# Kernel optimization log

Measured on AMD Instinct MI355X. Metric: run time of the kernel, lower is better.

## Reference

```python
import jax, jax.numpy as jnp
import numpy as np

N_NODES = 30000
N_EDGES = 240000
DIM = 128
HEADS = 2
HID = 2 * DIM          # gat1 per-head out channels = 256
OUT2 = DIM // 2        # gat2 per-head out channels = 64
CLASSES = 20
EPS = 1e-5
NEG_SLOPE = 0.2


def rmsnorm(x, w):
    x32 = x.astype(jnp.float32)
    y = x32 * jax.lax.rsqrt(jnp.mean(x32 * x32, axis=-1, keepdims=True) + EPS)
    return y.astype(x.dtype) * w


def gatv2_conv(x, src, dst, eattr, Wl, bl, Wr, br, We, att, bias, heads, ch):
    """PyG GATv2Conv (concat=True, add_self_loops=True, fill_value='mean')."""
    N = x.shape[0]
    # --- add self loops; self-loop edge_attr = per-node mean of incoming attrs ---
    cnt = jax.ops.segment_sum(jnp.ones((src.shape[0],), x.dtype), dst, num_segments=N)
    loop_attr = jax.ops.segment_sum(eattr, dst, num_segments=N) / jnp.maximum(cnt, 1.0)[:, None]
    loops = jnp.arange(N, dtype=src.dtype)
    src = jnp.concatenate([src, loops])
    dst = jnp.concatenate([dst, loops])
    eattr = jnp.concatenate([eattr, loop_attr], axis=0)
    # --- node transforms ---
    xl = (x @ Wl.T + bl).reshape(N, heads, ch)   # source-side
    xr = (x @ Wr.T + br).reshape(N, heads, ch)   # target-side
    eemb = (eattr @ We.T).reshape(-1, heads, ch)
    # --- edge-wise attention logits (GATv2: LeakyReLU before att dot) ---
    e = jax.nn.leaky_relu(xl[src] + xr[dst] + eemb, negative_slope=NEG_SLOPE)  # [E,H,C]
    logits = jnp.einsum('ehc,hc->eh', e, att)                                   # [E,H]
    # --- segment softmax over destination nodes ---
    m = jnp.full((N, heads), -jnp.inf, logits.dtype).at[dst].max(logits)
    p = jnp.exp(logits - m[dst])
    denom = jax.ops.segment_sum(p, dst, num_segments=N)
    alpha = p / denom[dst]                                                       # [E,H]
    # --- weighted scatter-add of source messages ---
    out = jax.ops.segment_sum(alpha[:, :, None] * xl[src], dst, num_segments=N)  # [N,H,C]
    return out.reshape(N, heads * ch) + bias


def setup_inputs() -> dict:
    key = jax.random.key(0)
    ks = jax.random.split(key, 20)
    d1 = HEADS * HID   # 512
    d2 = HEADS * OUT2  # 128 == DIM
    p = lambda k, shape: (jax.random.normal(k, shape, jnp.float32) * 0.02)
    return {
        'x': jax.random.normal(ks[0], (N_NODES, DIM), jnp.float32),
        'edge_index': jax.random.randint(ks[1], (2, N_EDGES), 0, N_NODES, jnp.int32),
        'edge_attr': jax.random.normal(ks[2], (N_EDGES, 1), jnp.float32),
        'Wl1': p(ks[3], (d1, DIM)), 'bl1': jnp.zeros((d1,), jnp.float32),
        'Wr1': p(ks[4], (d1, DIM)), 'br1': jnp.zeros((d1,), jnp.float32),
        'We1': p(ks[5], (d1, 1)),
        'att1': p(ks[6], (HEADS, HID)),
        'bias1': jnp.zeros((d1,), jnp.float32),
        'Wl2': p(ks[7], (d2, d1)), 'bl2': jnp.zeros((d2,), jnp.float32),
        'Wr2': p(ks[8], (d2, d1)), 'br2': jnp.zeros((d2,), jnp.float32),
        'We2': p(ks[9], (d2, 1)),
        'att2': p(ks[10], (HEADS, OUT2)),
        'bias2': jnp.zeros((d2,), jnp.float32),
        'w_ln1': jnp.ones((d1,), jnp.float32),
        'w_ln3': jnp.ones((d2,), jnp.float32),
        'W_out': p(ks[11], (CLASSES, d2)),
    }


def reference(x, edge_index, edge_attr,
              Wl1, bl1, Wr1, br1, We1, att1, bias1,
              Wl2, bl2, Wr2, br2, We2, att2, bias2,
              w_ln1, w_ln3, W_out):
    src, dst = edge_index[0], edge_index[1]
    h = gatv2_conv(x, src, dst, edge_attr, Wl1, bl1, Wr1, br1, We1, att1, bias1, HEADS, HID)
    h = jax.nn.silu(h)
    h = rmsnorm(h, w_ln1)
    h = gatv2_conv(h, src, dst, edge_attr, Wl2, bl2, Wr2, br2, We2, att2, bias2, HEADS, OUT2)
    h = rmsnorm(h, w_ln3)
    return h @ W_out.T
```

## Files before the change

kernel.cpp:

```cpp
#include <hip/hip_runtime.h>
#include <cstddef>

#define NN   30000
#define NNP  30016
#define NE   240000
#define D1   512
#define D2   128
#define NCLS 20
#define CAP  64
#define CAST_TOT 1025536
#define IDG_TOT  (CAST_TOT + NE)

typedef __attribute__((ext_vector_type(8))) short short8;
typedef __attribute__((ext_vector_type(4))) float f32x4;
typedef __attribute__((ext_vector_type(2))) float f32x2;

__device__ __forceinline__ unsigned short f2b(float f) {
  union { float f; unsigned int u; } c; c.f = f;
  unsigned int r = (c.u + 0x7fff + ((c.u >> 16) & 1)) >> 16;
  return (unsigned short)r;
}
__device__ __forceinline__ float b2f(unsigned short u) {
  union { unsigned int u; float f; } c; c.u = (unsigned int)u << 16;
  return c.f;
}
__device__ __forceinline__ f32x2 bpair(unsigned int t) {
  f32x2 r;
  r.x = __uint_as_float(t << 16);
  r.y = __uint_as_float(t & 0xffff0000u);
  return r;
}

__global__ __launch_bounds__(256) void k_build(
    const float* __restrict__ x,
    const float* __restrict__ Wl1, const float* __restrict__ Wr1,
    const float* __restrict__ Wl2, const float* __restrict__ Wr2,
    const int* __restrict__ src, const int* __restrict__ dst,
    const float* __restrict__ eattr,
    int* __restrict__ cnti,
    int2* __restrict__ se,
    unsigned short* __restrict__ xb,
    unsigned short* __restrict__ Wc1, unsigned short* __restrict__ Wc2) {
  int i = blockIdx.x * 256 + threadIdx.x;
  if (i >= IDG_TOT) return;
  if (i >= CAST_TOT) {
    int e = i - CAST_TOT;
    int d = dst[e];
    int pos = atomicAdd(&cnti[d], 1);
    if (pos < CAP) se[(size_t)d * CAP + pos] = make_int2(src[e], __float_as_int(eattr[e]));
    return;
  }
  const float* in; unsigned short* outp; int off;
  if      (i <  960000) { in = x;   outp = xb;          off = i; }
  else if (i <  976384) { in = Wl1; outp = Wc1;         off = i -  960000; }
  else if (i <  992768) { in = Wr1; outp = Wc1 + 65536; off = i -  976384; }
  else if (i < 1009152) { in = Wl2; outp = Wc2;         off = i -  992768; }
  else                  { in = Wr2; outp = Wc2 + 65536; off = i - 1009152; }
  float4 v = ((const float4*)in)[off];
  ushort4 o;
  o.x = f2b(v.x); o.y = f2b(v.y); o.z = f2b(v.z); o.w = f2b(v.w);
  ((ushort4*)outp)[off] = o;
}

template <int BN, int NT, int BK, int NBN>
__global__ __launch_bounds__(256) void gemm_mfma(
    const unsigned short* __restrict__ A, const unsigned short* __restrict__ W,
    const float* __restrict__ bl, const float* __restrict__ br, int Nhalf,
    unsigned short* __restrict__ Cl, unsigned short* __restrict__ Cr,
    int M, int N, int K) {
  constexpr int BM = 128, LDK = BK;
  constexpr int RPI = 512 / BK;
  constexpr int LPR = BK / 8;
  constexpr int CPAD = BN + 8;
  constexpr int SM_STAGE = BM * LDK + BN * LDK;
  constexpr int SM_C = BM * CPAD;
  constexpr int SMEM = SM_STAGE > SM_C ? SM_STAGE : SM_C;
  const int MBT = (M + BM - 1) / BM;
  {
  }
  const int id = blockIdx.x;
  const int g = id / (8 * NBN);
  const int rem = id % (8 * NBN);
  const int r8 = rem & 7;
  const int bnb = rem >> 3;
  const int bmb = g * 8 + r8;
  if (bmb >= MBT) return;
  __shared__ __align__(16) unsigned short smem[SMEM];
  unsigned short* As = smem;
  unsigned short* Bs = smem + BM * LDK;
  const int bm = bmb * BM;
  const int bn = bnb * BN;
  const int tid = threadIdx.x;
  const int lane = tid & 63;
  const int wid = __builtin_amdgcn_readfirstlane(tid >> 6);
  const int wm = (wid >> 1) * 64;
  const int wn = (wid & 1) * (NT * 16);
  const int l16 = lane & 15, lq = lane >> 4;
  const int lrow = lane / LPR;
  const int lcol = (lane % LPR) * 8;

  f32x4 acc[4][NT];
#pragma unroll
  for (int i = 0; i < 4; ++i)
#pragma unroll
    for (int j = 0; j < NT; ++j) acc[i][j] = (f32x4){0.f, 0.f, 0.f, 0.f};

  for (int k0 = 0; k0 < K; k0 += BK) {
#pragma unroll
    for (int p = 0; p < BM / (4 * RPI); ++p) {
      int r = p * (4 * RPI) + wid * RPI;
      const unsigned short* gp = A + (size_t)(bm + r + lrow) * K + k0 + lcol;
      __builtin_amdgcn_global_load_lds(
          (const __attribute__((address_space(1))) unsigned int*)gp,
          (__attribute__((address_space(3))) unsigned int*)(As + (size_t)r * LDK),
          16, 0, 0);
    }
#pragma unroll
    for (int p = 0; p < BN / (4 * RPI); ++p) {
      int r = p * (4 * RPI) + wid * RPI;
      const unsigned short* gp = W + (size_t)(bn + r + lrow) * K + k0 + lcol;
      __builtin_amdgcn_global_load_lds(
          (const __attribute__((address_space(1))) unsigned int*)gp,
          (__attribute__((address_space(3))) unsigned int*)(Bs + (size_t)r * LDK),
          16, 0, 0);
    }
    __syncthreads();
#pragma unroll
    for (int kh = 0; kh < BK / 32; ++kh) {
      short8 af[4], bfr[NT];
#pragma unroll
      for (int mt = 0; mt < 4; ++mt)
        af[mt] = *(const short8*)&As[(wm + mt * 16 + l16) * LDK + kh * 32 + lq * 8];
#pragma unroll
      for (int nt = 0; nt < NT; ++nt)
        bfr[nt] = *(const short8*)&Bs[(wn + nt * 16 + l16) * LDK + kh * 32 + lq * 8];
#pragma unroll
      for (int mt = 0; mt < 4; ++mt)
#pragma unroll
        for (int nt = 0; nt < NT; ++nt)
          acc[mt][nt] = __builtin_amdgcn_mfma_f32_16x16x32_bf16(
              af[mt], bfr[nt], acc[mt][nt], 0, 0, 0);
    }
    __syncthreads();
  }
  unsigned short* Cs = smem;
  const bool left = bn < Nhalf;
  const int ccb = left ? bn : bn - Nhalf;
  const float* bptr = left ? bl : br;
  unsigned short* Cp = left ? Cl : Cr;

#pragma unroll
  for (int nt = 0; nt < NT; ++nt) {
    int lc = wn + nt * 16 + l16;
    float b = bptr[ccb + lc];
#pragma unroll
    for (int mt = 0; mt < 4; ++mt)
#pragma unroll
      for (int r = 0; r < 4; ++r)
        Cs[(wm + mt * 16 + lq * 4 + r) * CPAD + lc] = f2b(acc[mt][nt][r] + b);
  }
  __syncthreads();
  constexpr int CHR = BN / 8;
  constexpr int NPASS = BM * CHR / 256;
#pragma unroll
  for (int p = 0; p < NPASS; ++p) {
    int c = p * 256 + tid;
    int row = c / CHR, col8 = (c % CHR) * 8;
    if (bm + row < M)
      *(short8*)&Cp[(size_t)(bm + row) * Nhalf + ccb + col8] =
          *(const short8*)&Cs[row * CPAD + col8];
  }
}

template <int D, int EPC, bool DO_SILU, bool OBF, bool HEAD_GEMM>
__global__ __launch_bounds__(256) void k_gat_node(
    const int2* __restrict__ se,
    const int* __restrict__ cnti,
    const unsigned short* __restrict__ xl, const unsigned short* __restrict__ xr,
    const float* __restrict__ We, const float* __restrict__ att,
    const float* __restrict__ bias, const float* __restrict__ w_ln,
    const float* __restrict__ Wout,
    unsigned short* __restrict__ outb, float* __restrict__ outf) {
  constexpr int VEC = D / 64;
  constexpr int PAIRS = VEC / 2;
  const int w = __builtin_amdgcn_readfirstlane(threadIdx.x) >> 6;
  const int n = blockIdx.x * 4 + w;
  const int lane = threadIdx.x & 63;
  const int c0 = lane * VEC;

  f32x2 xd2[PAIRS], we2[PAIRS], at2[PAIRS], acc2[PAIRS];
  {
    unsigned int tr[PAIRS];
    if constexpr (PAIRS == 4) {
      uint4 t = *(const uint4*)(xr + (size_t)n * D + c0);
      tr[0] = t.x; tr[1] = t.y; tr[2] = t.z; tr[3] = t.w;
    } else {
      tr[0] = *(const unsigned int*)(xr + (size_t)n * D + c0);
    }
    const f32x2* Wep = (const f32x2*)(We + c0);
    const f32x2* atp = (const f32x2*)(att + c0);
#pragma unroll
    for (int i = 0; i < PAIRS; i++) {
      xd2[i] = bpair(tr[i]);
      we2[i] = Wep[i];
      at2[i] = atp[i];
      acc2[i] = (f32x2){0.f, 0.f};
    }
  }

  const int start = n * CAP;
  const int deg = cnti[n];
  float denom = 0.f;
  float easum = 0.f;
  const int nfullE = deg / EPC;

  auto body = [&](const int (&s)[EPC], const float (&eav)[EPC], const float* wgt) {
    unsigned int uu[EPC][PAIRS];
#pragma unroll
    for (int k = 0; k < EPC; k++) {
      if constexpr (PAIRS == 4) {
        uint4 t = *(const uint4*)(xl + (size_t)s[k] * D + c0);
        uu[k][0] = t.x; uu[k][1] = t.y; uu[k][2] = t.z; uu[k][3] = t.w;
      } else {
        uu[k][0] = *(const unsigned int*)(xl + (size_t)s[k] * D + c0);
      }
    }
    f32x2 xs2[EPC][PAIRS];
    f32x2 p2[EPC];
#pragma unroll
    for (int j = 0; j < EPC; j++) p2[j] = (f32x2){0.f, 0.f};
#pragma unroll
    for (int i = 0; i < PAIRS; i++) {
#pragma unroll
      for (int j = 0; j < EPC; j++) {
        f32x2 xs = bpair(uu[j][i]);
        xs2[j][i] = xs;
        f32x2 ea = {eav[j], eav[j]};
        f32x2 q = __builtin_elementwise_fma(ea, we2[i], xd2[i]) + xs;
        f32x2 ql = __builtin_elementwise_max(q, q * 0.2f);
        p2[j] = __builtin_elementwise_fma(at2[i], ql, p2[j]);
      }
    }
    float p[EPC];
#pragma unroll
    for (int j = 0; j < EPC; j++) p[j] = p2[j].x + p2[j].y;
#pragma unroll
    for (int o = 16; o > 0; o >>= 1) {
#pragma unroll
      for (int j = 0; j < EPC; j++) p[j] += __shfl_xor(p[j], o);
    }
    float pe[EPC];
#pragma unroll
    for (int j = 0; j < EPC; j++) {
      pe[j] = __expf(p[j]);
      if (wgt) pe[j] *= wgt[j];
      denom += pe[j];
    }
#pragma unroll
    for (int i = 0; i < PAIRS; i++) {
#pragma unroll
      for (int j = 0; j < EPC; j++) {
        f32x2 pv = {pe[j], pe[j]};
        acc2[i] = __builtin_elementwise_fma(pv, xs2[j][i], acc2[i]);
      }
    }
  };

  for (int it = 0; it < nfullE; ++it) {
    int s[EPC]; float eav[EPC];
#pragma unroll
    for (int k = 0; k < EPC; k++) {
      int2 e = se[start + it * EPC + k];
      s[k] = e.x; eav[k] = __int_as_float(e.y);
      easum += eav[k];
    }
    body(s, eav, nullptr);
  }
  {
    const int base = nfullE * EPC;
    int s[EPC]; float eav[EPC]; float wgt[EPC];
#pragma unroll
    for (int k = 0; k < EPC; k++) {
      int idx = base + k;
      if (idx < deg) {
        int2 e = se[start + idx];
        s[k] = e.x; eav[k] = __int_as_float(e.y);
        easum += eav[k];
      }
    }
    float lan = easum / fmaxf((float)deg, 1.0f);
#pragma unroll
    for (int k = 0; k < EPC; k++) {
      int idx = base + k;
      if (idx >= deg) { s[k] = n; eav[k] = lan; }
      wgt[k] = (idx <= deg) ? 1.f : 0.f;
    }
    body(s, eav, wgt);
  }

  float inv = 1.f / denom;
  float vv[VEC], ss = 0.f;
#pragma unroll
  for (int i = 0; i < PAIRS; i++) {
#pragma unroll
    for (int h = 0; h < 2; h++) {
      int k = i * 2 + h;
      float v = fmaf(acc2[i][h], inv, bias[c0 + k]);
      if (DO_SILU) v = v / (1.f + __expf(-v));
      vv[k] = v;
      ss += v * v;
    }
  }
#pragma unroll
  for (int o = 32; o > 0; o >>= 1) ss += __shfl_xor(ss, o);
  float rinv = rsqrtf(ss / (float)D + 1e-5f);

  __shared__ __align__(16) float hrow[4][D2];
#pragma unroll
  for (int k = 0; k < VEC; k++) {
    float o = vv[k] * rinv * w_ln[c0 + k];
    if (OBF) outb[(size_t)n * D + c0 + k] = f2b(o);
    if (HEAD_GEMM) hrow[w][c0 + k] = o;
  }
  if (HEAD_GEMM) {
    __syncthreads();
    int t = threadIdx.x;
    if (t < 4 * NCLS) {
      int n4 = t / NCLS, c = t % NCLS;
      const float4* wr = (const float4*)(Wout + c * D2);
      const float4* hr = (const float4*)&hrow[n4][0];
      float sm = 0.f;
#pragma unroll
      for (int q = 0; q < D2 / 4; q++) {
        float4 a = hr[q], b = wr[q];
        sm += a.x * b.x + a.y * b.y + a.z * b.z + a.w * b.w;
      }
      outf[(size_t)(blockIdx.x * 4 + n4) * NCLS + c] = sm;
    }
  }
}

extern "C" void kernel_launch(void* const* d_in, const int* in_sizes, int n_in,
                              void* d_out, int out_size, void* d_ws, size_t ws_size,
                              hipStream_t stream) {
  const float* x     = (const float*)d_in[0];
  const int*   ei    = (const int*)  d_in[1];
  const float* eattr = (const float*)d_in[2];
  const float* Wl1   = (const float*)d_in[3];
  const float* bl1   = (const float*)d_in[4];
  const float* Wr1   = (const float*)d_in[5];
  const float* br1   = (const float*)d_in[6];
  const float* We1   = (const float*)d_in[7];
  const float* att1  = (const float*)d_in[8];
  const float* bias1 = (const float*)d_in[9];
  const float* Wl2   = (const float*)d_in[10];
  const float* bl2   = (const float*)d_in[11];
  const float* Wr2   = (const float*)d_in[12];
  const float* br2   = (const float*)d_in[13];
  const float* We2   = (const float*)d_in[14];
  const float* att2  = (const float*)d_in[15];
  const float* bias2 = (const float*)d_in[16];
  const float* w_ln1 = (const float*)d_in[17];
  const float* w_ln3 = (const float*)d_in[18];
  const float* W_out = (const float*)d_in[19];
  float* out = (float*)d_out;
  (void)in_sizes; (void)n_in; (void)out_size; (void)ws_size;

  const int* src = ei;
  const int* dst = ei + NE;

  char* wsp = (char*)d_ws;
  auto alloc = [&](size_t nbytes) {
    char* ptr = wsp;
    wsp += ((nbytes + 255) / 256) * 256;
    return ptr;
  };
  int*   cnti   = (int*)  alloc((size_t)NN * 4);
  int2*  se     = (int2*) alloc((size_t)NN * CAP * 8);
  unsigned short* xb   = (unsigned short*)alloc((size_t)NN * D2 * 2);
  unsigned short* Wc1  = (unsigned short*)alloc((size_t)2 * D1 * D2 * 2);
  unsigned short* Wc2  = (unsigned short*)alloc((size_t)2 * D2 * D1 * 2);
  unsigned short* xl1  = (unsigned short*)alloc((size_t)NN * D1 * 2);
  unsigned short* xr1  = (unsigned short*)alloc((size_t)NN * D1 * 2);
  unsigned short* h1b  = (unsigned short*)alloc((size_t)NN * D1 * 2);
  unsigned short* xl2  = (unsigned short*)alloc((size_t)NN * D2 * 2);
  unsigned short* xr2  = (unsigned short*)alloc((size_t)NN * D2 * 2);

  hipMemsetAsync(cnti, 0, (size_t)NNP * 4, stream);
  k_build<<<(IDG_TOT + 255) / 256, 256, 0, stream>>>(
      x, Wl1, Wr1, Wl2, Wr2, src, dst, eattr, cnti, se, xb, Wc1, Wc2);

  const int GB = NN / 4;
  const int G1 = 30 * 8 * 8;
  const int G2 = 30 * 8 * 2;

  gemm_mfma<128, 4, 64, 8><<<G1, 256, 0, stream>>>(
      xb, Wc1, bl1, br1, D1, xl1, xr1, NN, 2 * D1, D2);
  k_gat_node<D1, 4, true, true, false><<<GB, 256, 0, stream>>>(
      se, cnti, xl1, xr1, We1, att1, bias1, w_ln1, nullptr, h1b, nullptr);

  gemm_mfma<128, 4, 64, 2><<<G2, 256, 0, stream>>>(
      h1b, Wc2, bl2, br2, D2, xl2, xr2, NN, 2 * D2, D1);
  k_gat_node<D2, 8, false, false, true><<<GB, 256, 0, stream>>>(
      se, cnti, xl2, xr2, We2, att2, bias2, w_ln3, W_out, nullptr, out);
}
```

Before: 257.6 us.

## Move edge bucketing into first GEMM launch and zero counts in cast kernel

Replaces the hipMemsetAsync of the per-node counters with zeroing done inside the cast kernel. The atomic edge-bucketing work moves out of the cast kernel and into extra leading blocks of the first GEMM launch. This drops one launch and lets the scatter-heavy bucketing run alongside the MFMA GEMM tiles. The trade-off is that the bucketing blocks now compete with GEMM blocks for CUs, and the GEMM block indexing is offset by the number of bucketing blocks.

Measured after the change: 249.8 us. -3.0%, faster.

```diff
diff --git a/kernel.cpp b/kernel.cpp
--- a/kernel.cpp
+++ b/kernel.cpp
@@ -9,7 +9,9 @@
 #define NCLS 20
 #define CAP  64
 #define CAST_TOT 1025536
-#define IDG_TOT  (CAST_TOT + NE)
+#define ZERO_TOT (NNP / 4)
+#define KC_TOT  (CAST_TOT + ZERO_TOT)
+#define CSRB    ((NE + 255) / 256)
 
 typedef __attribute__((ext_vector_type(8))) short short8;
 typedef __attribute__((ext_vector_type(4))) float f32x4;
@@ -31,23 +33,17 @@
   return r;
 }
 
-__global__ __launch_bounds__(256) void k_build(
+__global__ __launch_bounds__(256) void k_cast(
     const float* __restrict__ x,
     const float* __restrict__ Wl1, const float* __restrict__ Wr1,
     const float* __restrict__ Wl2, const float* __restrict__ Wr2,
-    const int* __restrict__ src, const int* __restrict__ dst,
-    const float* __restrict__ eattr,
     int* __restrict__ cnti,
-    int2* __restrict__ se,
     unsigned short* __restrict__ xb,
     unsigned short* __restrict__ Wc1, unsigned short* __restrict__ Wc2) {
   int i = blockIdx.x * 256 + threadIdx.x;
-  if (i >= IDG_TOT) return;
+  if (i >= KC_TOT) return;
   if (i >= CAST_TOT) {
-    int e = i - CAST_TOT;
-    int d = dst[e];
-    int pos = atomicAdd(&cnti[d], 1);
-    if (pos < CAP) se[(size_t)d * CAP + pos] = make_int2(src[e], __float_as_int(eattr[e]));
+    ((int4*)cnti)[i - CAST_TOT] = make_int4(0, 0, 0, 0);
     return;
   }
   const float* in; unsigned short* outp; int off;
@@ -67,7 +63,10 @@
     const unsigned short* __restrict__ A, const unsigned short* __restrict__ W,
     const float* __restrict__ bl, const float* __restrict__ br, int Nhalf,
     unsigned short* __restrict__ Cl, unsigned short* __restrict__ Cr,
-    int M, int N, int K) {
+    int M, int N, int K,
+    int nCsrB, const int* __restrict__ esrc, const int* __restrict__ edst,
+    const float* __restrict__ eattr, int* __restrict__ cnti,
+    int2* __restrict__ sed) {
   constexpr int BM = 128, LDK = BK;
   constexpr int RPI = 512 / BK;
   constexpr int LPR = BK / 8;
@@ -76,11 +75,20 @@
   constexpr int SM_C = BM * CPAD;
   constexpr int SMEM = SM_STAGE > SM_C ? SM_STAGE : SM_C;
   const int MBT = (M + BM - 1) / BM;
-  {
-  }
   const int id = blockIdx.x;
-  const int g = id / (8 * NBN);
-  const int rem = id % (8 * NBN);
+  if (id < nCsrB) {
+    int e = id * 256 + threadIdx.x;
+    if (e < NE) {
+      int d = edst[e];
+      int pos = atomicAdd(&cnti[d], 1);
+      if (pos < CAP)
+        sed[(size_t)d * CAP + pos] = make_int2(esrc[e], __float_as_int(eattr[e]));
+    }
+    return;
+  }
+  const int gid = id - nCsrB;
+  const int g = gid / (8 * NBN);
+  const int rem = gid % (8 * NBN);
   const int r8 = rem & 7;
   const int bnb = rem >> 3;
   const int bmb = g * 8 + r8;
@@ -386,21 +394,22 @@
   unsigned short* xl2  = (unsigned short*)alloc((size_t)NN * D2 * 2);
   unsigned short* xr2  = (unsigned short*)alloc((size_t)NN * D2 * 2);
 
-  hipMemsetAsync(cnti, 0, (size_t)NNP * 4, stream);
-  k_build<<<(IDG_TOT + 255) / 256, 256, 0, stream>>>(
-      x, Wl1, Wr1, Wl2, Wr2, src, dst, eattr, cnti, se, xb, Wc1, Wc2);
+  k_cast<<<(KC_TOT + 255) / 256, 256, 0, stream>>>(
+      x, Wl1, Wr1, Wl2, Wr2, cnti, xb, Wc1, Wc2);
 
   const int GB = NN / 4;
   const int G1 = 30 * 8 * 8;
   const int G2 = 30 * 8 * 2;
 
-  gemm_mfma<128, 4, 64, 8><<<G1, 256, 0, stream>>>(
-      xb, Wc1, bl1, br1, D1, xl1, xr1, NN, 2 * D1, D2);
+  gemm_mfma<128, 4, 64, 8><<<CSRB + G1, 256, 0, stream>>>(
+      xb, Wc1, bl1, br1, D1, xl1, xr1, NN, 2 * D1, D2,
+      CSRB, src, dst, eattr, cnti, se);
   k_gat_node<D1, 4, true, true, false><<<GB, 256, 0, stream>>>(
       se, cnti, xl1, xr1, We1, att1, bias1, w_ln1, nullptr, h1b, nullptr);
 
   gemm_mfma<128, 4, 64, 2><<<G2, 256, 0, stream>>>(
-      h1b, Wc2, bl2, br2, D2, xl2, xr2, NN, 2 * D2, D1);
+      h1b, Wc2, bl2, br2, D2, xl2, xr2, NN, 2 * D2, D1,
+      0, src, dst, eattr, cnti, se);
   k_gat_node<D2, 8, false, false, true><<<GB, 256, 0, stream>>>(
       se, cnti, xl2, xr2, We2, att2, bias2, w_ln3, W_out, nullptr, out);
 }
```
